# Performance work log

Measured on AMD Instinct MI355X. Metric: run time of the kernel, lower is better.

## Reference

```python
import jax, jax.numpy as jnp
import numpy as np

K = 3
ALPHA = 8.3

def _patches(x, oh, ow):
    # x: [B, C, H, W] -> [B, C, K, K, oh, ow] (stride=1, dilation=1)
    rows = []
    for k in range(K):
        cols = [x[:, :, k:k + oh, l:l + ow] for l in range(K)]
        rows.append(jnp.stack(cols, axis=2))  # [B, C, K, oh, ow]
    return jnp.stack(rows, axis=2)  # [B, C, K, K, oh, ow]

def setup_inputs() -> dict:
    key = jax.random.key(0)
    k1, k2, k3, k4 = jax.random.split(key, 4)
    B, C, H, W = 4, 64, 256, 256
    OC = 64
    img = jax.random.normal(k1, (B, C, H, W), dtype=jnp.float32)
    depth = jax.random.uniform(k2, (B, 1, H, W), dtype=jnp.float32)
    weight = jax.random.uniform(k3, (OC, C, K, K), dtype=jnp.float32, minval=-0.1, maxval=0.1)
    bias = jax.random.uniform(k4, (1, OC), dtype=jnp.float32, minval=-0.1, maxval=0.1)
    return {"img": img, "depth": depth, "weight": weight, "bias": bias}

def reference(img, depth, weight, bias):
    B, C, H, W = img.shape
    oh, ow = H - K + 1, W - K + 1
    c0 = K // 2
    img_p = _patches(img, oh, ow)                 # [B, C, K, K, oh, ow]
    dep_p = _patches(depth, oh, ow)[:, 0]         # [B, K, K, oh, ow]
    center = depth[:, 0, c0:c0 + oh, c0:c0 + ow]  # [B, oh, ow]
    dw = jnp.exp(-ALPHA * jnp.abs(dep_p - center[:, None, None]))  # [B, K, K, oh, ow]
    out = jnp.einsum('bcklpq,bklpq,ockl->bopq', img_p, dw, weight)
    out = out + bias[0][None, :, None, None]
    return out
```

## Files before the change

### kernel.cpp

```cpp
#include <hip/hip_runtime.h>
#include <hip/hip_bf16.h>

typedef __bf16 bf16_t;
typedef __bf16 bf16x4 __attribute__((ext_vector_type(4)));
typedef __bf16 bf16x8 __attribute__((ext_vector_type(8)));
typedef float f32x4 __attribute__((ext_vector_type(4)));

#define ALPHA 8.3f
#define CPAD 72
#define NCOL 68


__global__ void repack_w(const float* __restrict__ w, bf16_t* __restrict__ w2) {
    int idx = blockIdx.x * 256 + threadIdx.x;
    if (idx >= 9 * 2 * 4 * 64 * 8) return;
    int j     = idx & 7;
    int lane  = (idx >> 3) & 63;
    int m     = (idx >> 9) & 3;
    int chunk = (idx >> 11) & 1;
    int tap   = idx >> 12;
    int oc = m * 16 + (lane & 15);
    int c  = chunk * 32 + (lane >> 4) * 8 + j;
    int kt = tap / 3, lt = tap % 3;
    w2[idx] = (bf16_t)w[((oc * 64 + c) * 3 + kt) * 3 + lt];
}

__global__ __launch_bounds__(256, 2) void depthconv_mfma(
    const float* __restrict__ img, const float* __restrict__ depth,
    const bf16_t* __restrict__ w2, const float* __restrict__ bias,
    float* __restrict__ out)
{
    __shared__ bf16_t lds[4 * NCOL * CPAD];

    const int tid = threadIdx.x;
    const int blk   = blockIdx.x;
    const int ppair = blk >> 4;
    const int r     = blk & 15;
    const int b     = r >> 2;
    const int qt    = r & 3;
    const int p0    = ppair * 2;
    const int q0    = (qt == 3) ? 190 : qt * 64;
    const int s0    = (qt == 3) ? 188 : q0;

    const float* imgb = img + (size_t)b * 64 * 65536;
    const float* dep  = depth + (size_t)b * 65536;

#pragma unroll
    for (int k = 0; k < 5; ++k) {
        int u = tid + (k << 8);
        if (u < 1088) {
            int cg   = u & 15;
            int rest = u >> 4;
            int colg = rest % 17;
            int row  = rest / 17;
            const float* src = imgb + (size_t)(cg * 4) * 65536 + (p0 + row) * 256 + s0 + colg * 4;
            f32x4 v0 = *(const f32x4*)src;
            f32x4 v1 = *(const f32x4*)(src + 65536);
            f32x4 v2 = *(const f32x4*)(src + 2 * 65536);
            f32x4 v3 = *(const f32x4*)(src + 3 * 65536);
            bf16_t* dst = lds + (size_t)(row * NCOL + colg * 4) * CPAD + cg * 4;
#pragma unroll
            for (int i = 0; i < 4; ++i)
                *(bf16x4*)(dst + i * CPAD) =
                    (bf16x4){(bf16_t)v0[i], (bf16_t)v1[i], (bf16_t)v2[i], (bf16_t)v3[i]};
        }
    }
    __syncthreads();

    const int wv   = tid >> 6;
    const int lane = tid & 63;
    const int pr   = wv >> 1;
    const int mh   = wv & 1;
    const int n    = lane & 15;
    const int quad = lane >> 4;
    const int prow = p0 + pr;
    const int clb0 = q0 - s0;

    float dc[4];
#pragma unroll
    for (int i = 0; i < 4; ++i)
        dc[i] = dep[(prow + 1) * 256 + q0 + 16 * i + n + 1];

    const f32x4 Z = (f32x4){0.f, 0.f, 0.f, 0.f};
    f32x4 acc[2][4];
#pragma unroll
    for (int mm = 0; mm < 2; ++mm)
#pragma unroll
        for (int i = 0; i < 4; ++i) acc[mm][i] = Z;

    for (int kt = 0; kt < 3; ++kt) {
        float dwv[3][4];
#pragma unroll
        for (int lt = 0; lt < 3; ++lt)
#pragma unroll
            for (int i = 0; i < 4; ++i) {
                float d = dep[(prow + kt) * 256 + q0 + 16 * i + n + lt];
                dwv[lt][i] = __expf(-ALPHA * fabsf(d - dc[i]));
            }
#pragma unroll
        for (int lt = 0; lt < 3; ++lt) {
            const int tap = kt * 3 + lt;
            const bf16x8* w2p = (const bf16x8*)w2 + ((size_t)(tap * 2) * 4 + mh * 2) * 64 + lane;
            bf16x8 a00 = w2p[0];
            bf16x8 a01 = w2p[64];
            bf16x8 a10 = w2p[256];
            bf16x8 a11 = w2p[256 + 64];
#pragma unroll
            for (int i = 0; i < 4; ++i) {
                const bf16_t* lp = lds
                    + (size_t)((pr + kt) * NCOL + clb0 + 16 * i + n + lt) * CPAD + quad * 8;
                const bf16x8 bf0 = *(const bf16x8*)lp;
                const bf16x8 bf1 = *(const bf16x8*)(lp + 32);
                f32x4 P0 = __builtin_amdgcn_mfma_f32_16x16x32_bf16(a00, bf0, Z, 0, 0, 0);
                f32x4 P1 = __builtin_amdgcn_mfma_f32_16x16x32_bf16(a01, bf0, Z, 0, 0, 0);
                P0 = __builtin_amdgcn_mfma_f32_16x16x32_bf16(a10, bf1, P0, 0, 0, 0);
                P1 = __builtin_amdgcn_mfma_f32_16x16x32_bf16(a11, bf1, P1, 0, 0, 0);
                acc[0][i] += dwv[lt][i] * P0;
                acc[1][i] += dwv[lt][i] * P1;
            }
        }
    }

#pragma unroll
    for (int mm = 0; mm < 2; ++mm) {
#pragma unroll
        for (int r2 = 0; r2 < 4; ++r2) {
            int oc = (mh * 2 + mm) * 16 + quad * 4 + r2;
            float bz = bias[oc];
#pragma unroll
            for (int i = 0; i < 4; ++i) {
                int q = q0 + 16 * i + n;
                out[((size_t)(b * 64 + oc) * 254 + prow) * 254 + q] = acc[mm][i][r2] + bz;
            }
        }
    }
}

extern "C" void kernel_launch(void* const* d_in, const int* in_sizes, int n_in,
                              void* d_out, int out_size, void* d_ws, size_t ws_size,
                              hipStream_t stream) {
    const float* img   = (const float*)d_in[0];
    const float* depth = (const float*)d_in[1];
    const float* w     = (const float*)d_in[2];
    const float* bias  = (const float*)d_in[3];
    bf16_t* w2 = (bf16_t*)d_ws;

    repack_w<<<144, 256, 0, stream>>>(w, w2);
    depthconv_mfma<<<2032, 256, 0, stream>>>(img, depth, w2, bias, (float*)d_out);
}
```

Measured before the change: 152.0 us.

## Warp-specialize producer/consumer with ring-buffered LDS rows over 8-row strips

Each block now covers a strip of 8 output rows instead of 2. Four producer waves stream image rows into a 6-slot LDS ring buffer while four consumer waves run the MFMA convolution, and the two groups hand off with raw s_barrier. This reuses the halo rows across consecutive row pairs and overlaps global loads with compute. In exchange it shrinks the grid to 512 blocks and adds a tight barrier handshake that could cause races or stalls. The last strip overlaps its neighbour, so some rows are written twice.

```diff
diff --git a/kernel.cpp b/kernel.cpp
--- a/kernel.cpp
+++ b/kernel.cpp
@@ -9,6 +9,7 @@
 #define ALPHA 8.3f
 #define CPAD 72
 #define NCOL 68
+#define NSLOT 6
 
 
 __global__ void repack_w(const float* __restrict__ w, bf16_t* __restrict__ w2) {
@@ -25,112 +26,159 @@
     w2[idx] = (bf16_t)w[((oc * 64 + c) * 3 + kt) * 3 + lt];
 }
 
-__global__ __launch_bounds__(256, 2) void depthconv_mfma(
+__global__ __launch_bounds__(512, 4) void depthconv_mfma(
     const float* __restrict__ img, const float* __restrict__ depth,
     const bf16_t* __restrict__ w2, const float* __restrict__ bias,
     float* __restrict__ out)
 {
-    __shared__ bf16_t lds[4 * NCOL * CPAD];
+    __shared__ bf16_t lds[NSLOT * NCOL * CPAD];
 
-    const int tid = threadIdx.x;
+    const int tid   = threadIdx.x;
     const int blk   = blockIdx.x;
-    const int ppair = blk >> 4;
+    const int strip = blk >> 4;
     const int r     = blk & 15;
     const int b     = r >> 2;
     const int qt    = r & 3;
-    const int p0    = ppair * 2;
+    const int prow0 = ((strip == 31) ? 123 : strip * 4) * 2;
     const int q0    = (qt == 3) ? 190 : qt * 64;
     const int s0    = (qt == 3) ? 188 : q0;
+    const int clb0  = q0 - s0;
 
     const float* imgb = img + (size_t)b * 64 * 65536;
     const float* dep  = depth + (size_t)b * 65536;
 
+    if (tid >= 256) {
+        const int ptid = tid - 256;
+        const int cgp  = ptid & 15;
+
 #pragma unroll
-    for (int k = 0; k < 5; ++k) {
-        int u = tid + (k << 8);
-        if (u < 1088) {
-            int cg   = u & 15;
-            int rest = u >> 4;
-            int colg = rest % 17;
-            int row  = rest / 17;
-            const float* src = imgb + (size_t)(cg * 4) * 65536 + (p0 + row) * 256 + s0 + colg * 4;
-            f32x4 v0 = *(const f32x4*)src;
-            f32x4 v1 = *(const f32x4*)(src + 65536);
-            f32x4 v2 = *(const f32x4*)(src + 2 * 65536);
-            f32x4 v3 = *(const f32x4*)(src + 3 * 65536);
-            bf16_t* dst = lds + (size_t)(row * NCOL + colg * 4) * CPAD + cg * 4;
+        for (int k = 0; k < 5; ++k) {
+            const int u = ptid + (k << 8);
+            if (u < 1088) {
+                const int rest = u >> 4;
+                const int colg = rest % 17, row = rest / 17;
+                const float* src = imgb + (size_t)(cgp * 4) * 65536
+                                 + (size_t)(prow0 + row) * 256 + s0 + colg * 4;
+                const f32x4 v0 = *(const f32x4*)src;
+                const f32x4 v1 = *(const f32x4*)(src + 65536);
+                const f32x4 v2 = *(const f32x4*)(src + 2 * 65536);
+                const f32x4 v3 = *(const f32x4*)(src + 3 * 65536);
+                bf16_t* dst = lds + (size_t)(row * NCOL + colg * 4) * CPAD + cgp * 4;
+#pragma unroll
+                for (int i = 0; i < 4; ++i)
+                    *(bf16x4*)(dst + i * CPAD) =
+                        (bf16x4){(bf16_t)v0[i], (bf16_t)v1[i], (bf16_t)v2[i], (bf16_t)v3[i]};
+            }
+        }
+        asm volatile("s_waitcnt lgkmcnt(0)" ::: "memory");
+        __builtin_amdgcn_s_barrier();
+
+#pragma unroll 1
+        for (int s = 1; s < 4; ++s) {
+            const int lb = 2 * s + 2;
+#pragma unroll
+            for (int k = 0; k < 3; ++k) {
+                const int u = ptid + (k << 8);
+                if (u < 544) {
+                    const int rest = u >> 4;
+                    const int colg = rest % 17, row = rest / 17;
+                    const int l    = lb + row;
+                    const int slot = (l >= NSLOT) ? l - NSLOT : l;
+                    const float* src = imgb + (size_t)(cgp * 4) * 65536
+                                     + (size_t)(prow0 + l) * 256 + s0 + colg * 4;
+                    const f32x4 v0 = *(const f32x4*)src;
+                    const f32x4 v1 = *(const f32x4*)(src + 65536);
+                    const f32x4 v2 = *(const f32x4*)(src + 2 * 65536);
+                    const f32x4 v3 = *(const f32x4*)(src + 3 * 65536);
+                    bf16_t* dst = lds + (size_t)(slot * NCOL + colg * 4) * CPAD + cgp * 4;
+#pragma unroll
+                    for (int i = 0; i < 4; ++i)
+                        *(bf16x4*)(dst + i * CPAD) =
+                            (bf16x4){(bf16_t)v0[i], (bf16_t)v1[i], (bf16_t)v2[i], (bf16_t)v3[i]};
+                }
+            }
+            asm volatile("s_waitcnt lgkmcnt(0)" ::: "memory");
+            __builtin_amdgcn_s_barrier();
+        }
+    } else {
+        const int wv   = tid >> 6;
+        const int lane = tid & 63;
+        const int pr   = wv >> 1;
+        const int mh   = wv & 1;
+        const int n    = lane & 15;
+        const int quad = lane >> 4;
+
+        const bf16x8* wbase = (const bf16x8*)w2 + (size_t)(mh * 2) * 64 + lane;
+        const f32x4 Z = (f32x4){0.f, 0.f, 0.f, 0.f};
+
+        __builtin_amdgcn_s_barrier();
+
+#pragma unroll 1
+        for (int s = 0; s < 4; ++s) {
+            const int prow = prow0 + 2 * s + pr;
+
+            float dc[4];
 #pragma unroll
             for (int i = 0; i < 4; ++i)
-                *(bf16x4*)(dst + i * CPAD) =
-                    (bf16x4){(bf16_t)v0[i], (bf16_t)v1[i], (bf16_t)v2[i], (bf16_t)v3[i]};
-        }
-    }
-    __syncthreads();
+                dc[i] = dep[(size_t)(prow + 1) * 256 + q0 + 16 * i + n + 1];
 
-    const int wv   = tid >> 6;
-    const int lane = tid & 63;
-    const int pr   = wv >> 1;
-    const int mh   = wv & 1;
-    const int n    = lane & 15;
-    const int quad = lane >> 4;
-    const int prow = p0 + pr;
-    const int clb0 = q0 - s0;
-
-    float dc[4];
+            f32x4 acc[2][4];
 #pragma unroll
-    for (int i = 0; i < 4; ++i)
-        dc[i] = dep[(prow + 1) * 256 + q0 + 16 * i + n + 1];
-
-    const f32x4 Z = (f32x4){0.f, 0.f, 0.f, 0.f};
-    f32x4 acc[2][4];
+            for (int mm = 0; mm < 2; ++mm)
 #pragma unroll
-    for (int mm = 0; mm < 2; ++mm)
-#pragma unroll
-        for (int i = 0; i < 4; ++i) acc[mm][i] = Z;
-
-    for (int kt = 0; kt < 3; ++kt) {
-        float dwv[3][4];
-#pragma unroll
-        for (int lt = 0; lt < 3; ++lt)
-#pragma unroll
-            for (int i = 0; i < 4; ++i) {
-                float d = dep[(prow + kt) * 256 + q0 + 16 * i + n + lt];
-                dwv[lt][i] = __expf(-ALPHA * fabsf(d - dc[i]));
-            }
-#pragma unroll
-        for (int lt = 0; lt < 3; ++lt) {
-            const int tap = kt * 3 + lt;
-            const bf16x8* w2p = (const bf16x8*)w2 + ((size_t)(tap * 2) * 4 + mh * 2) * 64 + lane;
-            bf16x8 a00 = w2p[0];
-            bf16x8 a01 = w2p[64];
-            bf16x8 a10 = w2p[256];
-            bf16x8 a11 = w2p[256 + 64];
-#pragma unroll
-            for (int i = 0; i < 4; ++i) {
-                const bf16_t* lp = lds
-                    + (size_t)((pr + kt) * NCOL + clb0 + 16 * i + n + lt) * CPAD + quad * 8;
-                const bf16x8 bf0 = *(const bf16x8*)lp;
-                const bf16x8 bf1 = *(const bf16x8*)(lp + 32);
-                f32x4 P0 = __builtin_amdgcn_mfma_f32_16x16x32_bf16(a00, bf0, Z, 0, 0, 0);
-                f32x4 P1 = __builtin_amdgcn_mfma_f32_16x16x32_bf16(a01, bf0, Z, 0, 0, 0);
-                P0 = __builtin_amdgcn_mfma_f32_16x16x32_bf16(a10, bf1, P0, 0, 0, 0);
-                P1 = __builtin_amdgcn_mfma_f32_16x16x32_bf16(a11, bf1, P1, 0, 0, 0);
-                acc[0][i] += dwv[lt][i] * P0;
-                acc[1][i] += dwv[lt][i] * P1;
-            }
-        }
-    }
+                for (int i = 0; i < 4; ++i) acc[mm][i] = Z;
 
 #pragma unroll
-    for (int mm = 0; mm < 2; ++mm) {
+            for (int kt = 0; kt < 3; ++kt) {
+                const int l    = 2 * s + pr + kt;
+                const int slot = (l >= NSLOT) ? l - NSLOT : l;
+                float dwv[3][4];
 #pragma unroll
-        for (int r2 = 0; r2 < 4; ++r2) {
-            int oc = (mh * 2 + mm) * 16 + quad * 4 + r2;
-            float bz = bias[oc];
+                for (int lt = 0; lt < 3; ++lt)
 #pragma unroll
-            for (int i = 0; i < 4; ++i) {
-                int q = q0 + 16 * i + n;
-                out[((size_t)(b * 64 + oc) * 254 + prow) * 254 + q] = acc[mm][i][r2] + bz;
+                    for (int i = 0; i < 4; ++i) {
+                        float d = dep[(size_t)(prow + kt) * 256 + q0 + 16 * i + n + lt];
+                        dwv[lt][i] = __expf(-ALPHA * fabsf(d - dc[i]));
+                    }
+#pragma unroll
+                for (int lt = 0; lt < 3; ++lt) {
+                    const int tap = kt * 3 + lt;
+                    const bf16x8* w2p = wbase + (size_t)tap * 512;
+                    const bf16x8 a00 = w2p[0];
+                    const bf16x8 a01 = w2p[64];
+                    const bf16x8 a10 = w2p[256];
+                    const bf16x8 a11 = w2p[320];
+#pragma unroll
+                    for (int i = 0; i < 4; ++i) {
+                        const bf16_t* lp = lds
+                            + (size_t)(slot * NCOL + clb0 + 16 * i + n + lt) * CPAD + quad * 8;
+                        const bf16x8 bf0 = *(const bf16x8*)lp;
+                        const bf16x8 bf1 = *(const bf16x8*)(lp + 32);
+                        f32x4 P0 = __builtin_amdgcn_mfma_f32_16x16x32_bf16(a00, bf0, Z, 0, 0, 0);
+                        f32x4 P1 = __builtin_amdgcn_mfma_f32_16x16x32_bf16(a01, bf0, Z, 0, 0, 0);
+                        P0 = __builtin_amdgcn_mfma_f32_16x16x32_bf16(a10, bf1, P0, 0, 0, 0);
+                        P1 = __builtin_amdgcn_mfma_f32_16x16x32_bf16(a11, bf1, P1, 0, 0, 0);
+                        acc[0][i] += dwv[lt][i] * P0;
+                        acc[1][i] += dwv[lt][i] * P1;
+                    }
+                }
+            }
+
+#pragma unroll
+            for (int mm = 0; mm < 2; ++mm)
+#pragma unroll
+                for (int r2 = 0; r2 < 4; ++r2) {
+                    const int oc = (mh * 2 + mm) * 16 + quad * 4 + r2;
+                    const float bz = bias[oc];
+#pragma unroll
+                    for (int i = 0; i < 4; ++i)
+                        out[((size_t)(b * 64 + oc) * 254 + prow) * 254 + q0 + 16 * i + n]
+                            = acc[mm][i][r2] + bz;
+                }
+
+            if (s < 3) {
+                asm volatile("s_waitcnt lgkmcnt(0)" ::: "memory");
+                __builtin_amdgcn_s_barrier();
             }
         }
     }
@@ -146,5 +194,5 @@
     bf16_t* w2 = (bf16_t*)d_ws;
 
     repack_w<<<144, 256, 0, stream>>>(w, w2);
-    depthconv_mfma<<<2032, 256, 0, stream>>>(img, depth, w2, bias, (float*)d_out);
+    depthconv_mfma<<<512, 512, 0, stream>>>(img, depth, w2, bias, (float*)d_out);
 }
```

After: 219.1 us. +44.1%, slower.

## Pre-transpose image to channel-last bf16 and read MFMA operands directly from global

Applied to the files above, without the earlier changes.

Adds a separate pass that converts the NCHW fp32 image into an NHWC bf16 buffer in workspace. The convolution kernel then loads its B operands straight from global memory (served by L1/L2) rather than staging a halo tile in LDS. This removes the per-block LDS staging, the conversion work and the barrier. The cost is an extra full-image write and read pass, plus uncached-style global loads in the inner loop. The old path is kept as a fallback for when the workspace is too small.

```diff
diff --git a/kernel.cpp b/kernel.cpp
--- a/kernel.cpp
+++ b/kernel.cpp
@@ -23,6 +23,113 @@
     int c  = chunk * 32 + (lane >> 4) * 8 + j;
     int kt = tap / 3, lt = tap % 3;
     w2[idx] = (bf16_t)w[((oc * 64 + c) * 3 + kt) * 3 + lt];
+}
+
+
+__global__ void transpose_img(const float* __restrict__ img, bf16_t* __restrict__ imgt) {
+    const int blk  = blockIdx.x;
+    const int wblk = blk & 3;
+    const int h    = (blk >> 2) & 255;
+    const int b    = blk >> 10;
+    const int tid  = threadIdx.x;
+    const int cg   = tid & 15;
+    const int colg = tid >> 4;
+    const float* src = img + (size_t)(b * 64 + cg * 4) * 65536 + h * 256 + wblk * 64 + colg * 4;
+    const f32x4 v0 = *(const f32x4*)src;
+    const f32x4 v1 = *(const f32x4*)(src + 65536);
+    const f32x4 v2 = *(const f32x4*)(src + 2 * 65536);
+    const f32x4 v3 = *(const f32x4*)(src + 3 * 65536);
+    bf16_t* dst = imgt + ((size_t)((b * 256 + h) * 256 + wblk * 64 + colg * 4)) * 64 + cg * 4;
+#pragma unroll
+    for (int i = 0; i < 4; ++i)
+        *(bf16x4*)(dst + (size_t)i * 64) =
+            (bf16x4){(bf16_t)v0[i], (bf16_t)v1[i], (bf16_t)v2[i], (bf16_t)v3[i]};
+}
+
+__global__ __launch_bounds__(256, 2) void depthconv_direct(
+    const float* __restrict__ depth, const bf16_t* __restrict__ w2,
+    const bf16_t* __restrict__ imgt, const float* __restrict__ bias,
+    float* __restrict__ out)
+{
+    const int blk   = blockIdx.x;
+    const int ppair = blk >> 4;
+    const int r     = blk & 15;
+    const int b     = r >> 2;
+    const int qt    = r & 3;
+    const int p0    = ppair * 2;
+    const int q0    = (qt == 3) ? 190 : qt * 64;
+
+    const float*  dep = depth + (size_t)b * 65536;
+    const bf16x8* tb  = (const bf16x8*)(imgt + (size_t)b * 64 * 65536);
+
+    const int tid  = threadIdx.x;
+    const int wv   = tid >> 6;
+    const int lane = tid & 63;
+    const int pr   = wv >> 1;
+    const int mh   = wv & 1;
+    const int n    = lane & 15;
+    const int quad = lane >> 4;
+    const int prow = p0 + pr;
+
+    float dc[4];
+#pragma unroll
+    for (int i = 0; i < 4; ++i)
+        dc[i] = dep[(size_t)(prow + 1) * 256 + q0 + 16 * i + n + 1];
+
+    const f32x4 Z = (f32x4){0.f, 0.f, 0.f, 0.f};
+    f32x4 acc[2][4];
+#pragma unroll
+    for (int mm = 0; mm < 2; ++mm)
+#pragma unroll
+        for (int i = 0; i < 4; ++i) acc[mm][i] = Z;
+
+    const bf16x8* wbase = (const bf16x8*)w2 + (size_t)(mh * 2) * 64 + lane;
+
+    for (int kt = 0; kt < 3; ++kt) {
+        float dwv[3][4];
+#pragma unroll
+        for (int lt = 0; lt < 3; ++lt)
+#pragma unroll
+            for (int i = 0; i < 4; ++i) {
+                float d = dep[(size_t)(prow + kt) * 256 + q0 + 16 * i + n + lt];
+                dwv[lt][i] = __expf(-ALPHA * fabsf(d - dc[i]));
+            }
+#pragma unroll
+        for (int lt = 0; lt < 3; ++lt) {
+            const int tap = kt * 3 + lt;
+            const bf16x8* w2p = wbase + (size_t)tap * 512;
+            const bf16x8 a00 = w2p[0];
+            const bf16x8 a01 = w2p[64];
+            const bf16x8 a10 = w2p[256];
+            const bf16x8 a11 = w2p[320];
+#pragma unroll
+            for (int i = 0; i < 4; ++i) {
+                const bf16x8* p = tb
+                    + ((size_t)(prow + kt) * 256 + (q0 + 16 * i + n + lt)) * 8 + quad;
+                const bf16x8 bf0 = p[0];
+                const bf16x8 bf1 = p[4];
+                f32x4 P0 = __builtin_amdgcn_mfma_f32_16x16x32_bf16(a00, bf0, Z, 0, 0, 0);
+                f32x4 P1 = __builtin_amdgcn_mfma_f32_16x16x32_bf16(a01, bf0, Z, 0, 0, 0);
+                P0 = __builtin_amdgcn_mfma_f32_16x16x32_bf16(a10, bf1, P0, 0, 0, 0);
+                P1 = __builtin_amdgcn_mfma_f32_16x16x32_bf16(a11, bf1, P1, 0, 0, 0);
+                acc[0][i] += dwv[lt][i] * P0;
+                acc[1][i] += dwv[lt][i] * P1;
+            }
+        }
+    }
+
+#pragma unroll
+    for (int mm = 0; mm < 2; ++mm) {
+#pragma unroll
+        for (int r2 = 0; r2 < 4; ++r2) {
+            const int oc = (mh * 2 + mm) * 16 + quad * 4 + r2;
+            const float bz = bias[oc];
+#pragma unroll
+            for (int i = 0; i < 4; ++i)
+                out[((size_t)(b * 64 + oc) * 254 + prow) * 254 + q0 + 16 * i + n]
+                    = acc[mm][i][r2] + bz;
+        }
+    }
 }
 
 __global__ __launch_bounds__(256, 2) void depthconv_mfma(
@@ -146,5 +253,14 @@
     bf16_t* w2 = (bf16_t*)d_ws;
 
     repack_w<<<144, 256, 0, stream>>>(w, w2);
-    depthconv_mfma<<<2032, 256, 0, stream>>>(img, depth, w2, bias, (float*)d_out);
-}
+
+    const size_t IMGT_OFF   = 131072;
+    const size_t IMGT_BYTES = (size_t)4 * 256 * 256 * 64 * 2;
+    if (ws_size >= IMGT_OFF + IMGT_BYTES) {
+        bf16_t* imgt = (bf16_t*)((char*)d_ws + IMGT_OFF);
+        transpose_img<<<4096, 256, 0, stream>>>(img, imgt);
+        depthconv_direct<<<2032, 256, 0, stream>>>(depth, w2, imgt, bias, (float*)d_out);
+    } else {
+        depthconv_mfma<<<2032, 256, 0, stream>>>(img, depth, w2, bias, (float*)d_out);
+    }
+}
```

Result: slower. 215.9 us (+42.0%).
